# Kernel tuning notes

Measured on AMD Instinct MI355X. Metric: run time of the kernel, lower is better.

Reference implementation:

```python
import math
import jax, jax.numpy as jnp
import numpy as np
from jax import lax

B, T, C = 2, 4096, 2048
N_HEAD, N_KV, D = 16, 4, 128
WINDOW, DILATION, CHUNK = 256, 1, 128


def make_rope_cache(seq_len, n_elem, base=10000.0):
    theta = 1.0 / base ** (jnp.arange(0, n_elem, 2, dtype=jnp.float32) / n_elem)
    idx_theta = jnp.arange(seq_len, dtype=jnp.float32)[:, None] * theta[None, :]
    return jnp.stack([jnp.cos(idx_theta), jnp.sin(idx_theta)], axis=-1)  # [T, n_elem/2, 2]


def setup_inputs() -> dict:
    key = jax.random.key(0)
    ks = jax.random.split(key, 5)
    s = 1.0 / math.sqrt(C)
    return {
        "x": jax.random.normal(ks[0], (B, T, C), dtype=jnp.float32),
        "wq": jax.random.normal(ks[1], (N_HEAD * D, C), dtype=jnp.float32) * s,
        "wk": jax.random.normal(ks[2], (N_KV * D, C), dtype=jnp.float32) * s,
        "wv": jax.random.normal(ks[3], (N_KV * D, C), dtype=jnp.float32) * s,
        "wo": jax.random.normal(ks[4], (N_HEAD * D, C), dtype=jnp.float32).T * s,  # stored [out,in]
        "rope_cache": make_rope_cache(T, D),
    }


def apply_rope(xh, cache):
    # xh: [B, T, H, D]; cache: [T, D/2, 2]
    b, t, h, d = xh.shape
    xr = xh.reshape(b, t, h, d // 2, 2)
    cos = cache[:t, :, 0][None, :, None, :]
    sin = cache[:t, :, 1][None, :, None, :]
    x0, x1 = xr[..., 0], xr[..., 1]
    rot = jnp.stack([x0 * cos - x1 * sin, x0 * sin + x1 * cos], axis=-1)
    return rot.reshape(b, t, h, d)


def sliding_attention(q, k, v, window, dilation, chunk):
    # q,k,v: [B, H, T, D] -> [B, H, T, D]; O(T*window), memory bounded via scan over chunks
    b, h, t, d = q.shape
    w = min(window, (t + dilation - 1) // dilation)
    offsets = jnp.arange(w) * dilation
    scale = 1.0 / math.sqrt(d)
    n_chunks = t // chunk

    def step(carry, c):
        pos = c * chunk + jnp.arange(chunk)                       # [L]
        idx_raw = (pos - (w - 1) * dilation)[:, None] + offsets[None, :]  # [L, w]
        invalid = idx_raw < 0
        idx = jnp.clip(idx_raw, 0, t - 1)
        flat = idx.reshape(-1)
        k_win = jnp.take(k, flat, axis=2).reshape(b, h, chunk, w, d)
        v_win = jnp.take(v, flat, axis=2).reshape(b, h, chunk, w, d)
        q_c = lax.dynamic_slice_in_dim(q, c * chunk, chunk, axis=2)
        scores = jnp.einsum('bhld,bhlwd->bhlw', q_c.astype(jnp.float32),
                            k_win.astype(jnp.float32)) * scale
        scores = jnp.where(invalid[None, None], -jnp.inf, scores)
        attn = jax.nn.softmax(scores, axis=-1)
        out_c = jnp.einsum('bhlw,bhlwd->bhld', attn, v_win.astype(jnp.float32))
        return carry, out_c.astype(q.dtype)

    _, outs = lax.scan(step, None, jnp.arange(n_chunks))  # [n_chunks, B, H, chunk, D]
    return outs.transpose(1, 2, 0, 3, 4).reshape(b, h, t, d)


def reference(x, wq, wk, wv, wo, rope_cache):
    b, t, c = x.shape
    q = (x @ wq.T).reshape(b, t, N_HEAD, D)
    k = (x @ wk.T).reshape(b, t, N_KV, D)
    v = (x @ wv.T).reshape(b, t, N_KV, D)
    q = apply_rope(q, rope_cache)
    k = apply_rope(k, rope_cache)
    q = q.transpose(0, 2, 1, 3)  # [B, H, T, D]
    k = k.transpose(0, 2, 1, 3)
    v = v.transpose(0, 2, 1, 3)
    g = N_HEAD // N_KV
    k = jnp.repeat(k, g, axis=1)
    v = jnp.repeat(v, g, axis=1)
    y = sliding_attention(q, k, v, WINDOW, DILATION, CHUNK)
    y = y.transpose(0, 2, 1, 3).reshape(b, t, c)
    return y @ wo.T
```

## Files before the change

### kernel.cpp

```cpp
#include <hip/hip_runtime.h>
#include <stdint.h>

typedef unsigned short u16;
typedef __attribute__((ext_vector_type(8))) short bf16x8;
typedef __attribute__((ext_vector_type(8))) unsigned short u16x8;
typedef __attribute__((ext_vector_type(4))) float f32x4;

#define B_  2
#define T_  4096
#define C_  2048
#define NH  16
#define NKV 4
#define HD  128

__device__ __forceinline__ u16 f2bf(float f) {
  union { float f; uint32_t u; } v; v.f = f;
  uint32_t u = v.u;
  u += 0x7fffu + ((u >> 16) & 1u);
  return (u16)(u >> 16);
}
__device__ __forceinline__ float bf2f(u16 h) {
  union { uint32_t u; float f; } v; v.u = ((uint32_t)h) << 16;
  return v.f;
}

__device__ __forceinline__ void gload_lds16(const u16* g, u16* l) {
  __builtin_amdgcn_global_load_lds(
      (const __attribute__((address_space(1))) void*)g,
      (__attribute__((address_space(3))) void*)l, 16, 0, 0);
}

__global__ void cvt_f32_bf16(const float* __restrict__ src, u16* __restrict__ dst, int n) {
  int i = (blockIdx.x * blockDim.x + threadIdx.x) * 4;
  if (i >= n) return;
  float4 v = *(const float4*)(src + i);
  ushort4 o;
  o.x = f2bf(v.x); o.y = f2bf(v.y); o.z = f2bf(v.z); o.w = f2bf(v.w);
  *(ushort4*)(dst + i) = o;
}

__global__ void rope_kernel(u16* __restrict__ qkv, const float* __restrict__ cache) {
  const int PH = (NH + NKV) * (HD / 2);
  long idx = (long)blockIdx.x * blockDim.x + threadIdx.x;
  if (idx >= (long)B_ * T_ * PH) return;
  int row = (int)(idx / PH);
  int rem = (int)(idx % PH);
  int hh = rem >> 6;
  int i  = rem & 63;
  int t  = row & (T_ - 1);
  float sc = (hh < NH) ? 0.1275174315f : 1.0f;
  float c = cache[t * 128 + 2 * i] * sc;
  float s = cache[t * 128 + 2 * i + 1] * sc;
  u16* p = qkv + (long)row * 3072 + hh * HD + 2 * i;
  float x0 = bf2f(p[0]), x1 = bf2f(p[1]);
  p[0] = f2bf(x0 * c - x1 * s);
  p[1] = f2bf(x0 * s + x1 * c);
}

__global__ void krearr(const u16* __restrict__ qkv, u16* __restrict__ K2) {
  int gid = blockIdx.x * 256 + threadIdx.x;
  int r = gid & 65535, bk = gid >> 16;
  int l16 = r & 15, q4 = (r >> 4) & 3, ks = (r >> 6) & 3, kb = r >> 8;
  int bb = bk >> 2, kv = bk & 3;
  const u16* src = qkv + ((long)(bb * T_ + kb * 16 + l16)) * 3072 + 2048 + kv * HD +
                   ks * 32 + q4 * 8;
  *(u16x8*)(K2 + (long)bk * 524288 + (long)r * 8) = *(const u16x8*)src;
}

__global__ void vrearr(const u16* __restrict__ qkv, u16* __restrict__ V2) {
  int gid = blockIdx.x * 256 + threadIdx.x;
  int r = gid & 65535, bk = gid >> 16;
  int l16 = r & 15, q4 = (r >> 4) & 3, ks = (r >> 6) & 3, jd = (r >> 8) & 7, kc = r >> 11;
  int bb = bk >> 2, kv = bk & 3;
  int key0 = kc * 128 + ks * 32 + q4 * 8;
  int d = jd * 16 + l16;
  const u16* src = qkv + ((long)(bb * T_ + key0)) * 3072 + 2560 + kv * HD + d;
  u16x8 v;
#pragma unroll
  for (int e = 0; e < 8; e++) v[e] = src[(long)e * 3072];
  *(u16x8*)(V2 + (long)bk * 524288 + (long)r * 8) = v;
}

#define GBAR() __builtin_amdgcn_s_barrier()

template <int WRITE_BF16>
__global__ __launch_bounds__(512, 2) void gemm256(const u16* __restrict__ A,
                                                  const u16* __restrict__ Bw,
                                                  void* __restrict__ Cv,
                                                  int M, int N, int K) {
  __shared__ u16 lds[65536];
  const int tid = threadIdx.x;
  const int lane = tid & 63;
  const int wave = tid >> 6;
  const int q4 = lane >> 4, l16 = lane & 15;
  const int wm = wave >> 2, wn = wave & 3;

  const int nwg = gridDim.x * gridDim.y;
  const int orig = blockIdx.y * gridDim.x + blockIdx.x;
  const int swz = (orig & 7) * (nwg >> 3) + (orig >> 3);
  const int bm = swz / gridDim.x, bn = swz % gridDim.x;
  const long m0 = (long)bm * 256, n0 = (long)bn * 256;

  const int srow = tid >> 2;
  const int slot = tid & 3;
  const int sx = (slot ^ ((srow >> 1) & 3)) * 8;
  const u16* Ag0 = A + (m0 + srow) * K + sx;
  const u16* Ag1 = A + (m0 + srow + 128) * K + sx;
  const u16* Bg0 = Bw + (n0 + srow) * K + sx;
  const u16* Bg1 = Bw + (n0 + srow + 128) * K + sx;
  u16* ldst = lds + tid * 8;

  const int nkt = K >> 6;

#define STAGE_A(bufi, kh, kt)                                  \
  do {                                                         \
    long ko = ((long)(kt) << 6) + ((kh) << 5);                 \
    u16* d = ldst + (bufi) * 32768 + (kh) * 8192;              \
    gload_lds16(Ag0 + ko, d);                                  \
    gload_lds16(Ag1 + ko, d + 4096);                           \
  } while (0)
#define STAGE_B(bufi, kh, kt)                                  \
  do {                                                         \
    long ko = ((long)(kt) << 6) + ((kh) << 5);                 \
    u16* d = ldst + (bufi) * 32768 + 16384 + (kh) * 8192;      \
    gload_lds16(Bg0 + ko, d);                                  \
    gload_lds16(Bg1 + ko, d + 4096);                           \
  } while (0)

  int offA[8], offB[4];
#pragma unroll
  for (int m = 0; m < 8; m++) {
    int r = wm * 128 + m * 16 + l16;
    offA[m] = r * 32 + ((q4 ^ ((r >> 1) & 3)) << 3);
  }
#pragma unroll
  for (int n = 0; n < 4; n++) {
    int r = wn * 64 + n * 16 + l16;
    offB[n] = 16384 + r * 32 + ((q4 ^ ((r >> 1) & 3)) << 3);
  }

  f32x4 acc[8][4] = {};

  STAGE_A(0, 0, 0); STAGE_B(0, 0, 0); STAGE_A(0, 1, 0); STAGE_B(0, 1, 0);
  if (nkt > 1) { STAGE_A(1, 0, 1); STAGE_B(1, 0, 1); }
  asm volatile("s_waitcnt vmcnt(4)" ::: "memory");
  GBAR();

  for (int kt = 0; kt < nkt; kt++) {
    const int bo = (kt & 1) * 32768;
    bf16x8 af[4], bfv[4];
#pragma unroll
    for (int m = 0; m < 4; m++) af[m] = *(const bf16x8*)(lds + bo + offA[m]);
#pragma unroll
    for (int n = 0; n < 4; n++) bfv[n] = *(const bf16x8*)(lds + bo + offB[n]);
    if (kt + 1 < nkt) STAGE_A((kt + 1) & 1, 1, kt + 1);
    GBAR();
    asm volatile("s_waitcnt lgkmcnt(0)" ::: "memory");
    __builtin_amdgcn_s_setprio(1);
#pragma unroll
    for (int m = 0; m < 4; m++)
#pragma unroll
      for (int n = 0; n < 4; n++)
        acc[m][n] = __builtin_amdgcn_mfma_f32_16x16x32_bf16(af[m], bfv[n], acc[m][n], 0, 0, 0);
    __builtin_amdgcn_s_setprio(0);
    GBAR();
#pragma unroll
    for (int m = 0; m < 4; m++) af[m] = *(const bf16x8*)(lds + bo + offA[4 + m]);
    if (kt + 1 < nkt) STAGE_B((kt + 1) & 1, 1, kt + 1);
    GBAR();
    asm volatile("s_waitcnt lgkmcnt(0)" ::: "memory");
    __builtin_amdgcn_s_setprio(1);
#pragma unroll
    for (int m = 0; m < 4; m++)
#pragma unroll
      for (int n = 0; n < 4; n++)
        acc[4 + m][n] = __builtin_amdgcn_mfma_f32_16x16x32_bf16(af[m], bfv[n], acc[4 + m][n], 0, 0, 0);
    __builtin_amdgcn_s_setprio(0);
    GBAR();
#pragma unroll
    for (int m = 0; m < 4; m++) af[m] = *(const bf16x8*)(lds + bo + 8192 + offA[m]);
#pragma unroll
    for (int n = 0; n < 4; n++) bfv[n] = *(const bf16x8*)(lds + bo + 8192 + offB[n]);
    if (kt + 2 < nkt) STAGE_A(kt & 1, 0, kt + 2);
    GBAR();
    asm volatile("s_waitcnt lgkmcnt(0)" ::: "memory");
    __builtin_amdgcn_s_setprio(1);
#pragma unroll
    for (int m = 0; m < 4; m++)
#pragma unroll
      for (int n = 0; n < 4; n++)
        acc[m][n] = __builtin_amdgcn_mfma_f32_16x16x32_bf16(af[m], bfv[n], acc[m][n], 0, 0, 0);
    __builtin_amdgcn_s_setprio(0);
    GBAR();
#pragma unroll
    for (int m = 0; m < 4; m++) af[m] = *(const bf16x8*)(lds + bo + 8192 + offA[4 + m]);
    if (kt + 2 < nkt) STAGE_B(kt & 1, 0, kt + 2);
    GBAR();
    asm volatile("s_waitcnt lgkmcnt(0)" ::: "memory");
    __builtin_amdgcn_s_setprio(1);
#pragma unroll
    for (int m = 0; m < 4; m++)
#pragma unroll
      for (int n = 0; n < 4; n++)
        acc[4 + m][n] = __builtin_amdgcn_mfma_f32_16x16x32_bf16(af[m], bfv[n], acc[4 + m][n], 0, 0, 0);
    __builtin_amdgcn_s_setprio(0);
    if (kt + 2 < nkt)
      asm volatile("s_waitcnt vmcnt(4)" ::: "memory");
    else
      asm volatile("s_waitcnt vmcnt(0)" ::: "memory");
    GBAR();
  }
#undef STAGE_A
#undef STAGE_B

  const long crow0 = m0 + wm * 128;
  const long ccol0 = n0 + wn * 64;
  if (WRITE_BF16) {
    u16* Cp = (u16*)Cv;
#pragma unroll
    for (int m = 0; m < 8; m++)
#pragma unroll
      for (int n = 0; n < 4; n++)
#pragma unroll
        for (int r = 0; r < 4; r++)
          Cp[(crow0 + m * 16 + q4 * 4 + r) * (long)N + ccol0 + n * 16 + l16] =
              f2bf(acc[m][n][r]);
  } else {
    float* Cp = (float*)Cv;
#pragma unroll
    for (int m = 0; m < 8; m++)
#pragma unroll
      for (int n = 0; n < 4; n++)
#pragma unroll
        for (int r = 0; r < 4; r++)
          Cp[(crow0 + m * 16 + q4 * 4 + r) * (long)N + ccol0 + n * 16 + l16] =
              acc[m][n][r];
  }
}

__global__ __launch_bounds__(256, 3) void attn_kernel(const u16* __restrict__ qkv,
                                                      const u16* __restrict__ K2,
                                                      const u16* __restrict__ V2,
                                                      u16* __restrict__ y) {
  const int tc = blockIdx.x, h = blockIdx.y, b = blockIdx.z;
  const int t0 = tc * 128;
  const int kvh = h >> 2;
  __shared__ u16 Pl[4 * 32 * 136];
  const int tid = threadIdx.x, wave = tid >> 6, lane = tid & 63;
  const int q4 = lane >> 4, l16 = lane & 15;
  u16* Pw = Pl + wave * (32 * 136);

  bf16x8 qf[2][4];
#pragma unroll
  for (int i = 0; i < 2; i++)
#pragma unroll
    for (int ks = 0; ks < 4; ks++)
      qf[i][ks] = *(const bf16x8*)(qkv +
          ((long)(b * T_ + t0 + 32 * wave + 16 * i + l16)) * 3072 + h * HD + ks * 32 + q4 * 8);

  f32x4 O[2][8] = {};
  float l_i[2][4] = {};

  const u16* Kb = K2 + (long)(b * NKV + kvh) * 524288 + lane * 8;
  const u16* Vb = V2 + (long)(b * NKV + kvh) * 524288 + lane * 8;

  int kstart = t0 - 256; if (kstart < 0) kstart = 0;
  for (int k0 = kstart; k0 <= t0; k0 += 128) {
    const u16* Kc = Kb + (long)(k0 >> 4) * 2048;
    const u16* Vc = Vb + (long)(k0 >> 7) * 16384;
    const int dbase0 = t0 + 32 * wave + q4 * 4 - k0 - l16;
    bf16x8 kn[4];
#pragma unroll
    for (int ks = 0; ks < 4; ks++) kn[ks] = *(const bf16x8*)(Kc + ks * 512);
#pragma unroll
    for (int j = 0; j < 8; j++) {
      bf16x8 kf[4];
#pragma unroll
      for (int ks = 0; ks < 4; ks++) kf[ks] = kn[ks];
      if (j < 7)
#pragma unroll
        for (int ks = 0; ks < 4; ks++)
          kn[ks] = *(const bf16x8*)(Kc + (j + 1) * 2048 + ks * 512);
      f32x4 s0 = {}, s1 = {};
#pragma unroll
      for (int ks = 0; ks < 4; ks++) {
        s0 = __builtin_amdgcn_mfma_f32_16x16x32_bf16(qf[0][ks], kf[ks], s0, 0, 0, 0);
        s1 = __builtin_amdgcn_mfma_f32_16x16x32_bf16(qf[1][ks], kf[ks], s1, 0, 0, 0);
      }
#pragma unroll
      for (int r = 0; r < 4; r++) {
        int d0 = dbase0 + r - 16 * j;
        float p0 = __builtin_amdgcn_exp2f(s0[r]);
        p0 = ((unsigned)d0 <= 255u) ? p0 : 0.f;
        l_i[0][r] += p0;
        Pw[(q4 * 4 + r) * 136 + 16 * j + l16] = f2bf(p0);
        int d1 = d0 + 16;
        float p1 = __builtin_amdgcn_exp2f(s1[r]);
        p1 = ((unsigned)d1 <= 255u) ? p1 : 0.f;
        l_i[1][r] += p1;
        Pw[(16 + q4 * 4 + r) * 136 + 16 * j + l16] = f2bf(p1);
      }
    }
    bf16x8 vn = *(const bf16x8*)(Vc);
#pragma unroll
    for (int ks = 0; ks < 4; ks++) {
      bf16x8 pf0 = *(const bf16x8*)(&Pw[l16 * 136 + ks * 32 + q4 * 8]);
      bf16x8 pf1 = *(const bf16x8*)(&Pw[(16 + l16) * 136 + ks * 32 + q4 * 8]);
#pragma unroll
      for (int jd = 0; jd < 8; jd++) {
        bf16x8 vf = vn;
        if (!(ks == 3 && jd == 7)) {
          int njd = (jd == 7) ? 0 : jd + 1;
          int nks = (jd == 7) ? ks + 1 : ks;
          vn = *(const bf16x8*)(Vc + (njd * 4 + nks) * 512);
        }
        O[0][jd] = __builtin_amdgcn_mfma_f32_16x16x32_bf16(pf0, vf, O[0][jd], 0, 0, 0);
        O[1][jd] = __builtin_amdgcn_mfma_f32_16x16x32_bf16(pf1, vf, O[1][jd], 0, 0, 0);
      }
    }
  }
#pragma unroll
  for (int d = 1; d < 16; d <<= 1)
#pragma unroll
    for (int i = 0; i < 2; i++)
#pragma unroll
      for (int r = 0; r < 4; r++)
        l_i[i][r] += __shfl_xor(l_i[i][r], d, 64);
#pragma unroll
  for (int i = 0; i < 2; i++)
#pragma unroll
    for (int r = 0; r < 4; r++) {
      float inv = 1.0f / l_i[i][r];
      long row = (long)(b * T_ + t0 + 32 * wave + 16 * i + q4 * 4 + r);
#pragma unroll
      for (int jd = 0; jd < 8; jd++)
        y[row * 2048 + h * HD + 16 * jd + l16] = f2bf(O[i][jd][r] * inv);
    }
}

extern "C" void kernel_launch(void* const* d_in, const int* in_sizes, int n_in,
                              void* d_out, int out_size, void* d_ws, size_t ws_size,
                              hipStream_t stream) {
  const float* x    = (const float*)d_in[0];
  const float* wq   = (const float*)d_in[1];
  const float* wk   = (const float*)d_in[2];
  const float* wv   = (const float*)d_in[3];
  const float* wo   = (const float*)d_in[4];
  const float* rope = (const float*)d_in[5];
  float* out = (float*)d_out;

  u16* xb   = (u16*)d_ws;
  u16* wqkv = xb + (long)8192 * 2048;
  u16* wob  = wqkv + (long)3072 * 2048;
  u16* qkv  = wob + (long)2048 * 2048;
  u16* V2   = qkv + (long)8192 * 3072;
  u16* K2   = wqkv;
  u16* yb   = xb;

  {
    long n = (long)8192 * 2048;
    cvt_f32_bf16<<<dim3((unsigned)((n / 4 + 255) / 256)), dim3(256), 0, stream>>>(x, xb, (int)n);
    n = (long)2048 * 2048;
    cvt_f32_bf16<<<dim3((unsigned)((n / 4 + 255) / 256)), dim3(256), 0, stream>>>(wq, wqkv, (int)n);
    n = (long)512 * 2048;
    cvt_f32_bf16<<<dim3((unsigned)((n / 4 + 255) / 256)), dim3(256), 0, stream>>>(
        wk, wqkv + (long)2048 * 2048, (int)n);
    cvt_f32_bf16<<<dim3((unsigned)((n / 4 + 255) / 256)), dim3(256), 0, stream>>>(
        wv, wqkv + (long)2048 * 2048 + (long)512 * 2048, (int)n);
    n = (long)2048 * 2048;
    cvt_f32_bf16<<<dim3((unsigned)((n / 4 + 255) / 256)), dim3(256), 0, stream>>>(wo, wob, (int)n);
  }

  gemm256<1><<<dim3(3072 / 256, 8192 / 256), dim3(512), 0, stream>>>(
      xb, wqkv, (void*)qkv, 8192, 3072, 2048);

  long npairs = (long)B_ * T_ * (NH + NKV) * (HD / 2);
  rope_kernel<<<dim3((unsigned)((npairs + 255) / 256)), dim3(256), 0, stream>>>(qkv, rope);

  krearr<<<dim3(2048), dim3(256), 0, stream>>>(qkv, K2);
  vrearr<<<dim3(2048), dim3(256), 0, stream>>>(qkv, V2);

  attn_kernel<<<dim3(T_ / 128, NH, B_), dim3(256), 0, stream>>>(qkv, K2, V2, yb);

  gemm256<0><<<dim3(2048 / 256, 8192 / 256), dim3(512), 0, stream>>>(
      yb, wob, (void*)out, 8192, 2048, 2048);
}
```

Baseline: 457.1 us.

## Software-pipeline LDS fragment loads with MFMAs and drop most barriers in GEMM

Restructures the GEMM inner loop so the LDS reads for the next MFMA block are issued before the current block's MFMAs run. It uses separate register sets (afX/afY, bvA/bvB) to double-buffer the fragments. Most per-phase workgroup barriers are removed, keeping one mid-iteration barrier and the end-of-iteration barrier, with sched_barrier fences after lgkmcnt waits. This targets barrier stalls and exposed LDS latency, at the cost of more VGPRs and a possible LDS write-after-read race if the stage-overwrite ordering is not guaranteed by the remaining barriers.

New measurement: 446.7 us. 1.02x faster.

```diff
diff --git a/kernel.cpp b/kernel.cpp
--- a/kernel.cpp
+++ b/kernel.cpp
@@ -82,6 +82,8 @@
 }
 
 #define GBAR() __builtin_amdgcn_s_barrier()
+#define LGKM0() do { asm volatile("s_waitcnt lgkmcnt(0)" ::: "memory"); \
+                     __builtin_amdgcn_sched_barrier(0); } while (0)
 
 template <int WRITE_BF16>
 __global__ __launch_bounds__(512, 2) void gemm256(const u16* __restrict__ A,
@@ -142,67 +144,65 @@
   f32x4 acc[8][4] = {};
 
   STAGE_A(0, 0, 0); STAGE_B(0, 0, 0); STAGE_A(0, 1, 0); STAGE_B(0, 1, 0);
-  if (nkt > 1) { STAGE_A(1, 0, 1); STAGE_B(1, 0, 1); }
-  asm volatile("s_waitcnt vmcnt(4)" ::: "memory");
+  if (nkt > 1) {
+    STAGE_A(1, 0, 1); STAGE_B(1, 0, 1);
+    asm volatile("s_waitcnt vmcnt(4)" ::: "memory");
+  } else {
+    asm volatile("s_waitcnt vmcnt(0)" ::: "memory");
+  }
   GBAR();
 
+  bf16x8 afX[4], afY[4], bvA[4], bvB[4];
   for (int kt = 0; kt < nkt; kt++) {
     const int bo = (kt & 1) * 32768;
-    bf16x8 af[4], bfv[4];
-#pragma unroll
-    for (int m = 0; m < 4; m++) af[m] = *(const bf16x8*)(lds + bo + offA[m]);
-#pragma unroll
-    for (int n = 0; n < 4; n++) bfv[n] = *(const bf16x8*)(lds + bo + offB[n]);
+#pragma unroll
+    for (int m = 0; m < 4; m++) afX[m] = *(const bf16x8*)(lds + bo + offA[m]);
+#pragma unroll
+    for (int n = 0; n < 4; n++) bvA[n] = *(const bf16x8*)(lds + bo + offB[n]);
     if (kt + 1 < nkt) STAGE_A((kt + 1) & 1, 1, kt + 1);
-    GBAR();
-    asm volatile("s_waitcnt lgkmcnt(0)" ::: "memory");
+    LGKM0();
+#pragma unroll
+    for (int m = 0; m < 4; m++) afY[m] = *(const bf16x8*)(lds + bo + offA[4 + m]);
     __builtin_amdgcn_s_setprio(1);
 #pragma unroll
     for (int m = 0; m < 4; m++)
 #pragma unroll
       for (int n = 0; n < 4; n++)
-        acc[m][n] = __builtin_amdgcn_mfma_f32_16x16x32_bf16(af[m], bfv[n], acc[m][n], 0, 0, 0);
+        acc[m][n] = __builtin_amdgcn_mfma_f32_16x16x32_bf16(afX[m], bvA[n], acc[m][n], 0, 0, 0);
+    __builtin_amdgcn_s_setprio(0);
+    if (kt + 1 < nkt) STAGE_B((kt + 1) & 1, 1, kt + 1);
+    LGKM0();
+#pragma unroll
+    for (int m = 0; m < 4; m++) afX[m] = *(const bf16x8*)(lds + bo + 8192 + offA[m]);
+#pragma unroll
+    for (int n = 0; n < 4; n++) bvB[n] = *(const bf16x8*)(lds + bo + 8192 + offB[n]);
+    __builtin_amdgcn_s_setprio(1);
+#pragma unroll
+    for (int m = 0; m < 4; m++)
+#pragma unroll
+      for (int n = 0; n < 4; n++)
+        acc[4 + m][n] = __builtin_amdgcn_mfma_f32_16x16x32_bf16(afY[m], bvA[n], acc[4 + m][n], 0, 0, 0);
     __builtin_amdgcn_s_setprio(0);
     GBAR();
-#pragma unroll
-    for (int m = 0; m < 4; m++) af[m] = *(const bf16x8*)(lds + bo + offA[4 + m]);
-    if (kt + 1 < nkt) STAGE_B((kt + 1) & 1, 1, kt + 1);
-    GBAR();
-    asm volatile("s_waitcnt lgkmcnt(0)" ::: "memory");
+    if (kt + 2 < nkt) STAGE_A(kt & 1, 0, kt + 2);
+    LGKM0();
+#pragma unroll
+    for (int m = 0; m < 4; m++) afY[m] = *(const bf16x8*)(lds + bo + 8192 + offA[4 + m]);
     __builtin_amdgcn_s_setprio(1);
 #pragma unroll
     for (int m = 0; m < 4; m++)
 #pragma unroll
       for (int n = 0; n < 4; n++)
-        acc[4 + m][n] = __builtin_amdgcn_mfma_f32_16x16x32_bf16(af[m], bfv[n], acc[4 + m][n], 0, 0, 0);
+        acc[m][n] = __builtin_amdgcn_mfma_f32_16x16x32_bf16(afX[m], bvB[n], acc[m][n], 0, 0, 0);
     __builtin_amdgcn_s_setprio(0);
-    GBAR();
-#pragma unroll
-    for (int m = 0; m < 4; m++) af[m] = *(const bf16x8*)(lds + bo + 8192 + offA[m]);
-#pragma unroll
-    for (int n = 0; n < 4; n++) bfv[n] = *(const bf16x8*)(lds + bo + 8192 + offB[n]);
-    if (kt + 2 < nkt) STAGE_A(kt & 1, 0, kt + 2);
-    GBAR();
-    asm volatile("s_waitcnt lgkmcnt(0)" ::: "memory");
+    if (kt + 2 < nkt) STAGE_B(kt & 1, 0, kt + 2);
+    LGKM0();
     __builtin_amdgcn_s_setprio(1);
 #pragma unroll
     for (int m = 0; m < 4; m++)
 #pragma unroll
       for (int n = 0; n < 4; n++)
-        acc[m][n] = __builtin_amdgcn_mfma_f32_16x16x32_bf16(af[m], bfv[n], acc[m][n], 0, 0, 0);
-    __builtin_amdgcn_s_setprio(0);
-    GBAR();
-#pragma unroll
-    for (int m = 0; m < 4; m++) af[m] = *(const bf16x8*)(lds + bo + 8192 + offA[4 + m]);
-    if (kt + 2 < nkt) STAGE_B(kt & 1, 0, kt + 2);
-    GBAR();
-    asm volatile("s_waitcnt lgkmcnt(0)" ::: "memory");
-    __builtin_amdgcn_s_setprio(1);
-#pragma unroll
-    for (int m = 0; m < 4; m++)
-#pragma unroll
-      for (int n = 0; n < 4; n++)
-        acc[4 + m][n] = __builtin_amdgcn_mfma_f32_16x16x32_bf16(af[m], bfv[n], acc[4 + m][n], 0, 0, 0);
+        acc[4 + m][n] = __builtin_amdgcn_mfma_f32_16x16x32_bf16(afY[m], bvB[n], acc[4 + m][n], 0, 0, 0);
     __builtin_amdgcn_s_setprio(0);
     if (kt + 2 < nkt)
       asm volatile("s_waitcnt vmcnt(4)" ::: "memory");
```
